# Performance work log

Hardware: AMD Instinct MI355X
Metric: run time of the kernel (lower is better)

## Reference

```python
import jax, jax.numpy as jnp
import numpy as np

N = 16384
D_IN = 64
D_OUT = 64


def setup_inputs() -> dict:
    key = jax.random.key(0)
    k_a, k_x, k_w = jax.random.split(key, 3)
    A = jax.random.uniform(k_a, (N, N), dtype=jnp.float32)  # dense weighted adjacency
    features = jax.random.normal(k_x, (N, D_IN), dtype=jnp.float32)
    weight = jax.random.normal(k_w, (D_IN, D_OUT), dtype=jnp.float32)
    bias = jnp.zeros((D_OUT,), dtype=jnp.float32)
    return {"A": A, "features": features, "weight": weight, "bias": bias}


def reference(A, features, weight, bias):
    # A_hat = A + I ; D = diag(colsum(A_hat)) ; A_norm = D^{-1} A_hat D^{-1}
    # Exploit diagonal D: two-sided scaling instead of inverse + dense matmuls.
    d_inv = 1.0 / (jnp.sum(A, axis=0) + 1.0)          # [N]
    xs = features * d_inv[:, None]                     # right-scale: D^{-1} x
    agg = (A @ xs + xs) * d_inv[:, None]               # (A + I) xs, then left-scale
    # dropout keep-prob = 1 - (1 - self.dropout) = 1.0 -> identity (dropout=1.0)
    return jax.nn.relu(agg @ weight + bias)
```

## Files before the change

kernel.cpp:

```cpp
#include <hip/hip_runtime.h>
#include <hip/hip_bf16.h>
#include <cstdint>
#include <cstddef>

#define N 16384
#define DF 64

typedef __attribute__((ext_vector_type(8))) short short8;
typedef __attribute__((ext_vector_type(4))) float f32x4;

__device__ __forceinline__ unsigned short f2bf(float f) {
    union { float f; uint32_t u; } v; v.f = f;
    uint32_t u = v.u;
    uint32_t r = u + 0x7fffu + ((u >> 16) & 1u);
    return (unsigned short)(r >> 16);
}

#define PROWS 64
__global__ __launch_bounds__(256) void colsum_kernel(const float* __restrict__ A,
                                                     float* __restrict__ partial) {
    int t = threadIdx.x;
    int c0 = blockIdx.x * 1024 + t * 4;
    int r0 = blockIdx.y * 256;
    const float* p = A + (size_t)r0 * N + c0;
    float ax = 0.f, ay = 0.f, az = 0.f, aw = 0.f;
    #pragma unroll 8
    for (int r = 0; r < 256; ++r) {
        float4 v = *(const float4*)(p + (size_t)r * N);
        ax += v.x; ay += v.y; az += v.z; aw += v.w;
    }
    float4 o; o.x = ax; o.y = ay; o.z = az; o.w = aw;
    *(float4*)&partial[(size_t)blockIdx.y * N + c0] = o;
}

__global__ __launch_bounds__(256) void prep_kernel(const float* __restrict__ feat,
                                                   const float* __restrict__ partial,
                                                   float* __restrict__ d_inv,
                                                   unsigned short* __restrict__ xsT) {
    __shared__ float tile[64][68];
    int t = threadIdx.x;
    int i0 = blockIdx.x * 64;
    int r = t >> 2;
    int q = t & 3;
    float s = 0.f;
    #pragma unroll
    for (int p = 0; p < 16; ++p)
        s += partial[(size_t)(q * 16 + p) * N + i0 + r];
    s += __shfl_xor(s, 1);
    s += __shfl_xor(s, 2);
    float dinv = 1.0f / (s + 1.0f);
    if (q == 0) d_inv[i0 + r] = dinv;

    int cq = q * 16;
    const float* fp = feat + (size_t)(i0 + r) * DF + cq;
    #pragma unroll
    for (int j = 0; j < 16; j += 4) {
        float4 v = *(const float4*)(fp + j);
        tile[r][cq + j + 0] = v.x * dinv;
        tile[r][cq + j + 1] = v.y * dinv;
        tile[r][cq + j + 2] = v.z * dinv;
        tile[r][cq + j + 3] = v.w * dinv;
    }
    __syncthreads();
    int c = t >> 2;
    int iq = (t & 3) * 16;
    short8 b0, b1;
    #pragma unroll
    for (int j = 0; j < 8; ++j) b0[j] = (short)f2bf(tile[iq + j][c]);
    #pragma unroll
    for (int j = 0; j < 8; ++j) b1[j] = (short)f2bf(tile[iq + 8 + j][c]);
    unsigned short* dst = xsT + (size_t)c * N + i0 + iq;
    *(short8*)(dst) = b0;
    *(short8*)(dst + 8) = b1;
}

#define KSPLIT 8
#define KCHUNK (N / KSPLIT)
#define BK 128
#define LDK 136

__global__ __launch_bounds__(256, 8) void gemm_kernel(const float* __restrict__ A,
                                                      const unsigned short* __restrict__ xsT,
                                                      float* __restrict__ agg) {
    __shared__ __align__(16) unsigned short xtile[64 * LDK];
    int t = threadIdx.x;
    int bid = blockIdx.x;
    int mb = bid >> 3;
    int ks = bid & 7;
    int m0 = mb * 64;
    int k0 = ks * KCHUNK;
    int w = t >> 6;
    int l = t & 63;
    int row = m0 + w * 16 + (l & 15);
    int kofs = (l >> 4) * 8;

    const float* arow = A + (size_t)row * N + k0 + kofs;

    f32x4 acc[4] = {};

    for (int kt = 0; kt < KCHUNK; kt += BK) {
        __syncthreads();
        #pragma unroll
        for (int i = 0; i < 4; ++i) {
            int ch = t + i * 256;
            int c = ch >> 4;
            int ko = (ch & 15) * 8;
            *(short8*)&xtile[c * LDK + ko] =
                *(const short8*)&xsT[(size_t)c * N + k0 + kt + ko];
        }
        __syncthreads();
        #pragma unroll
        for (int kk = 0; kk < BK; kk += 32) {
            float4 a0 = *(const float4*)(arow + kt + kk);
            float4 a1 = *(const float4*)(arow + kt + kk + 4);
            short8 af;
            af[0] = (short)f2bf(a0.x); af[1] = (short)f2bf(a0.y);
            af[2] = (short)f2bf(a0.z); af[3] = (short)f2bf(a0.w);
            af[4] = (short)f2bf(a1.x); af[5] = (short)f2bf(a1.y);
            af[6] = (short)f2bf(a1.z); af[7] = (short)f2bf(a1.w);
            #pragma unroll
            for (int ct = 0; ct < 4; ++ct) {
                short8 bf = *(const short8*)&xtile[(ct * 16 + (l & 15)) * LDK + kk + kofs];
                acc[ct] = __builtin_amdgcn_mfma_f32_16x16x32_bf16(af, bf, acc[ct], 0, 0, 0);
            }
        }
    }
    float* slab = agg + (size_t)ks * N * DF;
    int crow = m0 + w * 16 + (l >> 4) * 4;
    int ccol = l & 15;
    #pragma unroll
    for (int ct = 0; ct < 4; ++ct) {
        #pragma unroll
        for (int q = 0; q < 4; ++q)
            slab[(size_t)(crow + q) * DF + ct * 16 + ccol] = acc[ct][q];
    }
}

__global__ __launch_bounds__(256) void epilogue_kernel(const float* __restrict__ agg,
                                                       const float* __restrict__ feat,
                                                       const float* __restrict__ d_inv,
                                                       const float* __restrict__ W,
                                                       const float* __restrict__ bias,
                                                       float* __restrict__ out) {
    __shared__ float aggL[64][65];
    __shared__ float wL[64][64];
    int t = threadIdx.x;
    int i0 = blockIdx.x * 64;
    int r = t >> 2;
    int cq = (t & 3) * 16;
    {
        const float* wp = W + r * 64 + cq;
        #pragma unroll
        for (int j = 0; j < 16; j += 4) {
            float4 v = *(const float4*)(wp + j);
            wL[r][cq + j + 0] = v.x; wL[r][cq + j + 1] = v.y;
            wL[r][cq + j + 2] = v.z; wL[r][cq + j + 3] = v.w;
        }
    }
    float dinv = d_inv[i0 + r];
    const float* fp = feat + (size_t)(i0 + r) * DF + cq;
    size_t base = (size_t)(i0 + r) * DF + cq;
    #pragma unroll
    for (int j = 0; j < 16; j += 4) {
        float4 fv = *(const float4*)(fp + j);
        float sx = fv.x * dinv, sy = fv.y * dinv, sz = fv.z * dinv, sw = fv.w * dinv;
        #pragma unroll
        for (int sl = 0; sl < KSPLIT; ++sl) {
            float4 a = *(const float4*)(agg + (size_t)sl * N * DF + base + j);
            sx += a.x; sy += a.y; sz += a.z; sw += a.w;
        }
        aggL[r][cq + j + 0] = sx * dinv;
        aggL[r][cq + j + 1] = sy * dinv;
        aggL[r][cq + j + 2] = sz * dinv;
        aggL[r][cq + j + 3] = sw * dinv;
    }
    __syncthreads();
    int k = t & 63;
    int rg = t >> 6;
    float bk = bias[k];
    for (int it = 0; it < 16; ++it) {
        int rr = rg * 16 + it;
        float acc = bk;
        #pragma unroll
        for (int c = 0; c < 64; ++c) acc += aggL[rr][c] * wL[c][k];
        out[(size_t)(i0 + rr) * DF + k] = fmaxf(acc, 0.0f);
    }
}

extern "C" void kernel_launch(void* const* d_in, const int* in_sizes, int n_in,
                              void* d_out, int out_size, void* d_ws, size_t ws_size,
                              hipStream_t stream) {
    const float* A    = (const float*)d_in[0];
    const float* feat = (const float*)d_in[1];
    const float* W    = (const float*)d_in[2];
    const float* bias = (const float*)d_in[3];
    float* out = (float*)d_out;

    float* ws = (float*)d_ws;
    float* partial = ws;
    float* agg     = ws + (size_t)PROWS * N;
    float* dinv    = agg + (size_t)KSPLIT * N * DF;
    unsigned short* xsT = (unsigned short*)(dinv + N);

    colsum_kernel<<<dim3(16, 64), 256, 0, stream>>>(A, partial);
    prep_kernel<<<N / 64, 256, 0, stream>>>(feat, partial, dinv, xsT);
    gemm_kernel<<<(N / 64) * KSPLIT, 256, 0, stream>>>(A, xsT, agg);
    epilogue_kernel<<<N / 64, 256, 0, stream>>>(agg, feat, dinv, W, bias, out);
}
```

Baseline: 430.9 us.

## Fuse bf16 conversion of A into colsum pass and reverse gemm row order

The column-sum pass now also writes a bf16 copy of A to workspace using nontemporal loads, and the GEMM reads that half-size copy instead of converting fp32 on the fly. GEMM row blocks are processed in reverse order so recently written rows may still be in the last-level cache. This removes in-loop conversion and halves GEMM read bytes, but adds a 512 MiB write and a large workspace requirement.

```diff
diff --git a/kernel.cpp b/kernel.cpp
--- a/kernel.cpp
+++ b/kernel.cpp
@@ -17,20 +17,33 @@
 }
 
 #define PROWS 64
-__global__ __launch_bounds__(256) void colsum_kernel(const float* __restrict__ A,
-                                                     float* __restrict__ partial) {
-    int t = threadIdx.x;
-    int c0 = blockIdx.x * 1024 + t * 4;
+__global__ __launch_bounds__(256) void colsum_convert_kernel(const float* __restrict__ A,
+                                                             unsigned short* __restrict__ A16,
+                                                             float* __restrict__ partial) {
+    int t = threadIdx.x;
+    int c0 = blockIdx.x * 2048 + t * 8;
     int r0 = blockIdx.y * 256;
     const float* p = A + (size_t)r0 * N + c0;
-    float ax = 0.f, ay = 0.f, az = 0.f, aw = 0.f;
-    #pragma unroll 8
+    unsigned short* q = A16 + (size_t)r0 * N + c0;
+    float s0 = 0.f, s1 = 0.f, s2 = 0.f, s3 = 0.f;
+    float s4 = 0.f, s5 = 0.f, s6 = 0.f, s7 = 0.f;
+    #pragma unroll 4
     for (int r = 0; r < 256; ++r) {
-        float4 v = *(const float4*)(p + (size_t)r * N);
-        ax += v.x; ay += v.y; az += v.z; aw += v.w;
-    }
-    float4 o; o.x = ax; o.y = ay; o.z = az; o.w = aw;
-    *(float4*)&partial[(size_t)blockIdx.y * N + c0] = o;
+        f32x4 v0 = __builtin_nontemporal_load((const f32x4*)(p + (size_t)r * N));
+        f32x4 v1 = __builtin_nontemporal_load((const f32x4*)(p + (size_t)r * N + 4));
+        s0 += v0.x; s1 += v0.y; s2 += v0.z; s3 += v0.w;
+        s4 += v1.x; s5 += v1.y; s6 += v1.z; s7 += v1.w;
+        short8 o;
+        o[0] = (short)f2bf(v0.x); o[1] = (short)f2bf(v0.y);
+        o[2] = (short)f2bf(v0.z); o[3] = (short)f2bf(v0.w);
+        o[4] = (short)f2bf(v1.x); o[5] = (short)f2bf(v1.y);
+        o[6] = (short)f2bf(v1.z); o[7] = (short)f2bf(v1.w);
+        *(short8*)(q + (size_t)r * N) = o;
+    }
+    float4 o0; o0.x = s0; o0.y = s1; o0.z = s2; o0.w = s3;
+    float4 o1; o1.x = s4; o1.y = s5; o1.z = s6; o1.w = s7;
+    *(float4*)&partial[(size_t)blockIdx.y * N + c0] = o0;
+    *(float4*)&partial[(size_t)blockIdx.y * N + c0 + 4] = o1;
 }
 
 __global__ __launch_bounds__(256) void prep_kernel(const float* __restrict__ feat,
@@ -79,22 +92,24 @@
 #define BK 128
 #define LDK 136
 
-__global__ __launch_bounds__(256, 8) void gemm_kernel(const float* __restrict__ A,
+__global__ __launch_bounds__(256, 8) void gemm_kernel(const unsigned short* __restrict__ A16,
                                                       const unsigned short* __restrict__ xsT,
                                                       float* __restrict__ agg) {
     __shared__ __align__(16) unsigned short xtile[64 * LDK];
     int t = threadIdx.x;
     int bid = blockIdx.x;
-    int mb = bid >> 3;
+    int mb = 255 - (bid >> 3);
     int ks = bid & 7;
     int m0 = mb * 64;
     int k0 = ks * KCHUNK;
     int w = t >> 6;
     int l = t & 63;
-    int row = m0 + w * 16 + (l & 15);
-    int kofs = (l >> 4) * 8;
-
-    const float* arow = A + (size_t)row * N + k0 + kofs;
+    int fr = l & 15;
+    int fq = l >> 4;
+    int row = m0 + w * 16 + fr;
+    int kofs = fq * 8;
+
+    const unsigned short* arow = A16 + (size_t)row * N + k0 + kofs;
 
     f32x4 acc[4] = {};
 
@@ -103,24 +118,18 @@
         #pragma unroll
         for (int i = 0; i < 4; ++i) {
             int ch = t + i * 256;
-            int c = ch >> 4;
+            int f = ch >> 4;
             int ko = (ch & 15) * 8;
-            *(short8*)&xtile[c * LDK + ko] =
-                *(const short8*)&xsT[(size_t)c * N + k0 + kt + ko];
+            *(short8*)&xtile[f * LDK + ko] =
+                *(const short8*)&xsT[(size_t)f * N + k0 + kt + ko];
         }
         __syncthreads();
         #pragma unroll
         for (int kk = 0; kk < BK; kk += 32) {
-            float4 a0 = *(const float4*)(arow + kt + kk);
-            float4 a1 = *(const float4*)(arow + kt + kk + 4);
-            short8 af;
-            af[0] = (short)f2bf(a0.x); af[1] = (short)f2bf(a0.y);
-            af[2] = (short)f2bf(a0.z); af[3] = (short)f2bf(a0.w);
-            af[4] = (short)f2bf(a1.x); af[5] = (short)f2bf(a1.y);
-            af[6] = (short)f2bf(a1.z); af[7] = (short)f2bf(a1.w);
+            short8 af = *(const short8*)(arow + kt + kk);
             #pragma unroll
             for (int ct = 0; ct < 4; ++ct) {
-                short8 bf = *(const short8*)&xtile[(ct * 16 + (l & 15)) * LDK + kk + kofs];
+                short8 bf = *(const short8*)&xtile[(ct * 16 + fr) * LDK + kk + kofs];
                 acc[ct] = __builtin_amdgcn_mfma_f32_16x16x32_bf16(af, bf, acc[ct], 0, 0, 0);
             }
         }
@@ -196,14 +205,14 @@
     const float* bias = (const float*)d_in[3];
     float* out = (float*)d_out;
 
-    float* ws = (float*)d_ws;
-    float* partial = ws;
-    float* agg     = ws + (size_t)PROWS * N;
+    unsigned short* A16 = (unsigned short*)d_ws;
+    float* partial = (float*)(A16 + (size_t)N * N);
+    float* agg     = partial + (size_t)PROWS * N;
     float* dinv    = agg + (size_t)KSPLIT * N * DF;
     unsigned short* xsT = (unsigned short*)(dinv + N);
 
-    colsum_kernel<<<dim3(16, 64), 256, 0, stream>>>(A, partial);
+    colsum_convert_kernel<<<dim3(8, 64), 256, 0, stream>>>(A, A16, partial);
     prep_kernel<<<N / 64, 256, 0, stream>>>(feat, partial, dinv, xsT);
-    gemm_kernel<<<(N / 64) * KSPLIT, 256, 0, stream>>>(A, xsT, agg);
+    gemm_kernel<<<(N / 64) * KSPLIT, 256, 0, stream>>>(A16, xsT, agg);
     epilogue_kernel<<<N / 64, 256, 0, stream>>>(agg, feat, dinv, W, bias, out);
 }
```

After: 525.3 us. +21.9%, slower.
